# Kernel optimization log

Hardware: AMD Instinct MI355X
Metric: run time of the kernel (lower is better)

## Reference

```python
import jax, jax.numpy as jnp
import numpy as np
import itertools

N = 65536          # points
R = 1.0 / 16.0     # radius (forward uses 1/16)
K = 64             # max_num_neighbors in forward call
G = 16             # grid cells per axis (cell size == R)


def _radius_knn_edges(pts):
    """Grid-hashed radius search; per point keep nearest K within R (self-loop included),
    pad with self index so every point has exactly K edges (max-aggregation neutral)."""
    cells = np.minimum((pts / R).astype(np.int64), G - 1)
    cid = (cells[:, 0] * G + cells[:, 1]) * G + cells[:, 2]
    order = np.argsort(cid, kind='stable')
    sorted_cid = cid[order]
    counts = np.bincount(cid, minlength=G ** 3)
    starts = np.concatenate([[0], np.cumsum(counts)[:-1]])
    M = int(counts.max())
    cand = -np.ones((G ** 3, M), dtype=np.int64)
    slot = np.arange(N) - starts[sorted_cid]
    cand[sorted_cid, slot] = order
    offs = np.array(list(itertools.product([-1, 0, 1], repeat=3)))
    nbr = np.empty((N, K), dtype=np.int64)
    chunk = 4096
    for s in range(0, N, chunk):
        e = min(s + chunk, N)
        c = cells[s:e]
        nc = c[:, None, :] + offs[None]                      # [B,27,3]
        valid_c = np.all((nc >= 0) & (nc < G), axis=-1)      # [B,27]
        ncid = (nc[..., 0] * G + nc[..., 1]) * G + nc[..., 2]
        ncid = np.where(valid_c, ncid, 0)
        cd = cand[ncid]                                      # [B,27,M]
        cd = np.where(np.broadcast_to(valid_c[..., None], cd.shape), cd, -1)
        cd = cd.reshape(e - s, -1)                           # [B,27M]
        p = pts[np.maximum(cd, 0)]
        d = np.linalg.norm(p - pts[s:e, None, :], axis=-1)
        d = np.where((cd >= 0) & (d <= R), d, np.inf)
        sel = np.argsort(d, axis=1)[:, :K]
        row = np.arange(e - s)[:, None]
        picked = cd[row, sel]
        ok = np.isfinite(d[row, sel])
        nbr[s:e] = np.where(ok, picked, np.arange(s, e)[:, None])
    out_index = np.repeat(np.arange(N, dtype=np.int64), K)
    in_index = nbr.reshape(-1)
    return out_index, in_index


def setup_inputs() -> dict:
    key = jax.random.key(0)
    ks = jax.random.split(key, 16)
    pos = jax.random.uniform(ks[0], (N, 3), dtype=jnp.float32)
    rgb = jax.random.uniform(ks[1], (N, 3), dtype=jnp.float32)
    batch = jnp.zeros((N,), dtype=jnp.int64)
    oi, ii = _radius_knn_edges(np.asarray(pos, dtype=np.float64))
    out_index = jnp.asarray(oi)
    in_index = jnp.asarray(ii)

    def lin_w(k, fi, fo):
        return jax.random.normal(k, (fi, fo), dtype=jnp.float32) / np.sqrt(fi).astype(np.float32)

    def lin_b(k, fo):
        return 0.01 * jax.random.normal(k, (fo,), dtype=jnp.float32)

    return {
        'pos': pos, 'rgb': rgb, 'batch': batch,
        'out_index': out_index, 'in_index': in_index,
        'w1a': lin_w(ks[2], 6, 8),   'b1a': lin_b(ks[3], 8),
        'w1b': lin_w(ks[4], 8, 8),   'b1b': lin_b(ks[5], 8),
        'w2a': lin_w(ks[6], 11, 16), 'b2a': lin_b(ks[7], 16),
        'w2b': lin_w(ks[8], 16, 16), 'b2b': lin_b(ks[9], 16),
        'w3a': lin_w(ks[10], 19, 32), 'b3a': lin_b(ks[11], 32),
        'w3b': lin_w(ks[12], 32, 32), 'b3b': lin_b(ks[13], 32),
    }


def _point_conv(x, pos, out_index, in_index, wa, ba, wb, bb):
    # gather neighbor features + relative position, local MLP, max-scatter, output linear
    dpos = pos[in_index] - pos[out_index]                      # [E,3]
    msg = jnp.concatenate([x[in_index], dpos], axis=-1)        # [E,c_in+3]
    h = jax.nn.celu(msg @ wa + ba)                             # [E,c_mid]
    agg = jax.ops.segment_max(h, out_index, num_segments=pos.shape[0],
                              indices_are_sorted=True)         # [N,c_mid]
    return agg @ wb + bb                                       # [N,c_out]


def reference(pos, rgb, batch, out_index, in_index,
              w1a, b1a, w1b, b1b, w2a, b2a, w2b, b2b, w3a, b3a, w3b, b3b):
    out = jax.nn.celu(_point_conv(pos, pos, out_index, in_index, w1a, b1a, w1b, b1b))
    out = jax.nn.celu(_point_conv(out, pos, out_index, in_index, w2a, b2a, w2b, b2b))
    out = jax.nn.celu(_point_conv(out, pos, out_index, in_index, w3a, b3a, w3b, b3b))
    return (pos, out, batch)
```

## Files before the change

kernel.cpp:

```cpp
#include <hip/hip_runtime.h>
#include <hip/hip_fp16.h>
#include <math.h>


#define NPTS 65536
#define KNBR 64
#define TILE 32
#define NCELL 4096

__device__ __forceinline__ float celu1(float x) {
    return x > 0.0f ? x : (__expf(x) - 1.0f);
}

__device__ __forceinline__ unsigned pkmax(unsigned a, unsigned b) {
    unsigned d;
    asm("v_pk_max_f16 %0, %1, %2" : "=v"(d) : "v"(a), "v"(b));
    return d;
}

__device__ __forceinline__ unsigned pack2(float a, float b) {
    __half2 h = __floats2half2_rn(a, b);
    return *(unsigned*)&h;
}


__global__ __launch_bounds__(256) void k_cell(
    const float* __restrict__ pos, float* __restrict__ dout, int out_size,
    int* __restrict__ cid, int* __restrict__ hist)
{
    int t = blockIdx.x * 256 + threadIdx.x;
    if (t < NPTS) {
        float p0 = pos[3 * t + 0];
        float p1 = pos[3 * t + 1];
        float p2 = pos[3 * t + 2];
        dout[3 * t + 0] = p0;
        dout[3 * t + 1] = p1;
        dout[3 * t + 2] = p2;
        int cx = min((int)(p0 * 16.0f), 15);
        int cy = min((int)(p1 * 16.0f), 15);
        int cz = min((int)(p2 * 16.0f), 15);
        int c = (cx * 16 + cy) * 16 + cz;
        cid[t] = c;
        atomicAdd(&hist[c], 1);
        for (int j = 35 * NPTS + t; j < out_size; j += NPTS)
            dout[j] = 0.0f;
    }
}

__global__ __launch_bounds__(64) void k_scan(
    const int* __restrict__ hist, int* __restrict__ cellptr)
{
    int l = threadIdx.x;
    int v[64];
    int s = 0;
#pragma unroll
    for (int i = 0; i < 64; ++i) { v[i] = s; s += hist[l * 64 + i]; }
    int run = s;
#pragma unroll
    for (int st = 1; st < 64; st <<= 1) {
        int o = __shfl_up(run, st, 64);
        if (l >= st) run += o;
    }
    int off = run - s;
#pragma unroll
    for (int i = 0; i < 64; ++i)
        cellptr[l * 64 + i] = off + v[i];
}

__global__ __launch_bounds__(256) void k_scatter(
    const float* __restrict__ pos, const int* __restrict__ cid,
    int* __restrict__ cellptr, unsigned short* __restrict__ perm,
    int* __restrict__ order, float* __restrict__ pos_s,
    const float* __restrict__ w1a, const float* __restrict__ b1a,
    __half* __restrict__ q1s)
{
    int t = blockIdx.x * 256 + threadIdx.x;
    if (t >= NPTS) return;
    int c = cid[t];
    int nid = atomicAdd(&cellptr[c], 1);
    perm[t] = (unsigned short)nid;
    order[nid] = t;
    float p0 = pos[3 * t + 0];
    float p1 = pos[3 * t + 1];
    float p2 = pos[3 * t + 2];
    pos_s[3 * nid + 0] = p0;
    pos_s[3 * nid + 1] = p1;
    pos_s[3 * nid + 2] = p2;
    float q[8];
#pragma unroll
    for (int ch = 0; ch < 8; ++ch) {
        float a = b1a[ch];
        a = fmaf(p0, w1a[0 * 8 + ch] + w1a[3 * 8 + ch], a);
        a = fmaf(p1, w1a[1 * 8 + ch] + w1a[4 * 8 + ch], a);
        a = fmaf(p2, w1a[2 * 8 + ch] + w1a[5 * 8 + ch], a);
        q[ch] = a;
    }
    uint4 pk;
    pk.x = pack2(q[0], q[1]);
    pk.y = pack2(q[2], q[3]);
    pk.z = pack2(q[4], q[5]);
    pk.w = pack2(q[6], q[7]);
    *(uint4*)(q1s + 8 * nid) = pk;
}

__global__ __launch_bounds__(256) void k_trans(
    const int* __restrict__ idx, const int* __restrict__ order,
    const unsigned short* __restrict__ perm, unsigned short* __restrict__ idxs)
{
    int g = blockIdx.x * 256 + threadIdx.x;
    int row = g >> 3;
    int j = g & 7;
    int old = order[row];
    const int4* src = (const int4*)(idx + old * KNBR + j * 8);
    int4 v0 = src[0];
    int4 v1 = src[1];
    uint4 o;
    o.x = (unsigned)perm[v0.x] | ((unsigned)perm[v0.y] << 16);
    o.y = (unsigned)perm[v0.z] | ((unsigned)perm[v0.w] << 16);
    o.z = (unsigned)perm[v1.x] | ((unsigned)perm[v1.y] << 16);
    o.w = (unsigned)perm[v1.z] | ((unsigned)perm[v1.w] << 16);
    *(uint4*)(idxs + row * KNBR + j * 8) = o;
}

template <int FH, int FOUT, int FHN, bool WRITEX>
__global__ __launch_bounds__(256, 8) void k_layer(
    const __half* __restrict__ q,
    const unsigned short* __restrict__ idx,
    const float* __restrict__ pos,
    const int* __restrict__ order,
    const float* __restrict__ wap,
    const float* __restrict__ wb,
    const float* __restrict__ bb,
    const float* __restrict__ wan,
    const float* __restrict__ ban,
    float* __restrict__ xout,
    __half* __restrict__ qnext)
{
    constexpr int SL  = FH / 8;
    constexpr int LPP = SL * 8;
    constexpr int PPW = 64 / LPP;
    constexpr int NIT = TILE / (4 * PPW);

    __shared__ uint4 m_lds[TILE * SL];

    int w  = threadIdx.x >> 6;
    int l  = threadIdx.x & 63;
    int pl = l / LPP;
    int u  = l % LPP;
    int c  = u % SL;
    int g  = u / SL;
    int tb = (blockIdx.x & 255) * (NPTS / TILE / 256) + (blockIdx.x >> 8);
    int pbase = tb * TILE;

#pragma unroll
    for (int it = 0; it < NIT; ++it) {
        int lp = it * (4 * PPW) + w * PPW + pl;
        int p  = pbase + lp;
        uint4 iv = *(const uint4*)(idx + p * KNBR + g * 8);
        int e0 = iv.x & 0xffff, e1 = iv.x >> 16;
        int e2 = iv.y & 0xffff, e3 = iv.y >> 16;
        int e4 = iv.z & 0xffff, e5 = iv.z >> 16;
        int e6 = iv.w & 0xffff, e7 = iv.w >> 16;
        uint4 v[8];
        v[0] = *(const uint4*)(q + e0 * FH + c * 8);
        v[1] = *(const uint4*)(q + e1 * FH + c * 8);
        v[2] = *(const uint4*)(q + e2 * FH + c * 8);
        v[3] = *(const uint4*)(q + e3 * FH + c * 8);
        v[4] = *(const uint4*)(q + e4 * FH + c * 8);
        v[5] = *(const uint4*)(q + e5 * FH + c * 8);
        v[6] = *(const uint4*)(q + e6 * FH + c * 8);
        v[7] = *(const uint4*)(q + e7 * FH + c * 8);

        unsigned ax = 0xFC00FC00u, ay = 0xFC00FC00u, az = 0xFC00FC00u, aw = 0xFC00FC00u;
#pragma unroll
        for (int k = 0; k < 8; ++k) {
            ax = pkmax(ax, v[k].x);
            ay = pkmax(ay, v[k].y);
            az = pkmax(az, v[k].z);
            aw = pkmax(aw, v[k].w);
        }
#pragma unroll
        for (int st = SL; st < LPP; st <<= 1) {
            ax = pkmax(ax, (unsigned)__shfl_xor((int)ax, st, 64));
            ay = pkmax(ay, (unsigned)__shfl_xor((int)ay, st, 64));
            az = pkmax(az, (unsigned)__shfl_xor((int)az, st, 64));
            aw = pkmax(aw, (unsigned)__shfl_xor((int)aw, st, 64));
        }
        if (g == 0) {
            uint4 r; r.x = ax; r.y = ay; r.z = az; r.w = aw;
            m_lds[lp * SL + c] = r;
        }
    }
    __syncthreads();

    if constexpr (WRITEX) {
        if (threadIdx.x < TILE * 4) {
            int pt  = threadIdx.x >> 2;
            int qtr = threadIdx.x & 3;
            int p   = pbase + pt;
            float p0 = pos[3 * p + 0];
            float p1 = pos[3 * p + 1];
            float p2 = pos[3 * p + 2];

            float h[FH];
#pragma unroll
            for (int s = 0; s < SL; ++s) {
                uint4 vv = m_lds[pt * SL + s];
                unsigned w4[4] = {vv.x, vv.y, vv.z, vv.w};
#pragma unroll
                for (int k = 0; k < 4; ++k) {
                    float2 f = __half22float2(*(__half2*)&w4[k]);
                    h[s * 8 + k * 2 + 0] = f.x;
                    h[s * 8 + k * 2 + 1] = f.y;
                }
            }
#pragma unroll
            for (int ch = 0; ch < FH; ++ch) {
                float gg = p0 * wap[ch] + p1 * wap[FH + ch] + p2 * wap[2 * FH + ch];
                h[ch] = celu1(h[ch] - gg);
            }
            float x[8];
#pragma unroll
            for (int j = 0; j < 8; ++j) {
                int c2 = qtr * 8 + j;
                float a = bb[c2];
#pragma unroll
                for (int ch = 0; ch < FH; ++ch)
                    a = fmaf(h[ch], wb[ch * FOUT + c2], a);
                x[j] = celu1(a);
            }
            int oldp = order[p];
            float4* xo = (float4*)(xout + (long long)oldp * FOUT + qtr * 8);
            xo[0] = make_float4(x[0], x[1], x[2], x[3]);
            xo[1] = make_float4(x[4], x[5], x[6], x[7]);
        }
    } else if (threadIdx.x < TILE) {
        int lt = threadIdx.x;
        int p  = pbase + lt;
        float p0 = pos[3 * p + 0];
        float p1 = pos[3 * p + 1];
        float p2 = pos[3 * p + 2];

        float h[FH];
#pragma unroll
        for (int s = 0; s < SL; ++s) {
            uint4 vv = m_lds[lt * SL + s];
            unsigned w4[4] = {vv.x, vv.y, vv.z, vv.w};
#pragma unroll
            for (int k = 0; k < 4; ++k) {
                float2 f = __half22float2(*(__half2*)&w4[k]);
                h[s * 8 + k * 2 + 0] = f.x;
                h[s * 8 + k * 2 + 1] = f.y;
            }
        }
#pragma unroll
        for (int ch = 0; ch < FH; ++ch) {
            float gg = p0 * wap[ch] + p1 * wap[FH + ch] + p2 * wap[2 * FH + ch];
            h[ch] = celu1(h[ch] - gg);
        }
        float x[FOUT];
#pragma unroll
        for (int c2 = 0; c2 < FOUT; ++c2) {
            float a = bb[c2];
#pragma unroll
            for (int ch = 0; ch < FH; ++ch)
                a = fmaf(h[ch], wb[ch * FOUT + c2], a);
            x[c2] = celu1(a);
        }
        if constexpr (FHN > 0) {
            uint4* qo = (uint4*)(qnext + p * FHN);
#pragma unroll
            for (int s = 0; s < FHN / 8; ++s) {
                float qn[8];
#pragma unroll
                for (int k = 0; k < 8; ++k) {
                    int cn = s * 8 + k;
                    float a = ban[cn];
#pragma unroll
                    for (int c2 = 0; c2 < FOUT; ++c2)
                        a = fmaf(x[c2], wan[c2 * FHN + cn], a);
                    a = fmaf(p0, wan[(FOUT + 0) * FHN + cn], a);
                    a = fmaf(p1, wan[(FOUT + 1) * FHN + cn], a);
                    a = fmaf(p2, wan[(FOUT + 2) * FHN + cn], a);
                    qn[k] = a;
                }
                uint4 pk;
                pk.x = pack2(qn[0], qn[1]);
                pk.y = pack2(qn[2], qn[3]);
                pk.z = pack2(qn[4], qn[5]);
                pk.w = pack2(qn[6], qn[7]);
                qo[s] = pk;
            }
        }
    }
}

extern "C" void kernel_launch(void* const* d_in, const int* in_sizes, int n_in,
                              void* d_out, int out_size, void* d_ws, size_t ws_size,
                              hipStream_t stream) {
    const float* pos = (const float*)d_in[0];
    const int* idx = (const int*)d_in[4];
    const float* w1a = (const float*)d_in[5];
    const float* b1a = (const float*)d_in[6];
    const float* w1b = (const float*)d_in[7];
    const float* b1b = (const float*)d_in[8];
    const float* w2a = (const float*)d_in[9];
    const float* b2a = (const float*)d_in[10];
    const float* w2b = (const float*)d_in[11];
    const float* b2b = (const float*)d_in[12];
    const float* w3a = (const float*)d_in[13];
    const float* b3a = (const float*)d_in[14];
    const float* w3b = (const float*)d_in[15];
    const float* b3b = (const float*)d_in[16];
    float* out = (float*)d_out;

    char* ws = (char*)d_ws;
    __half* A      = (__half*)ws;
    __half* B      = (__half*)(ws + (4u << 20));
    unsigned short* idxs = (unsigned short*)(ws + (6u << 20));
    int*    cid    = (int*)(ws + (14u << 20));
    int*    order  = (int*)(ws + (14u << 20) + (256u << 10));
    unsigned short* perm = (unsigned short*)(ws + (14u << 20) + (512u << 10));
    int*    hist   = (int*)(ws + (14u << 20) + (640u << 10));
    int*    cellptr= (int*)(ws + (14u << 20) + (656u << 10));
    float*  pos_s  = (float*)(ws + (15u << 20));

    hipMemsetAsync(hist, 0, NCELL * sizeof(int), stream);
    k_cell<<<NPTS / 256, 256, 0, stream>>>(pos, out, out_size, cid, hist);
    k_scan<<<1, 64, 0, stream>>>(hist, cellptr);
    k_scatter<<<NPTS / 256, 256, 0, stream>>>(pos, cid, cellptr, perm, order,
                                              pos_s, w1a, b1a, A);
    k_trans<<<NPTS * 8 / 256, 256, 0, stream>>>(idx, order, perm, idxs);

    k_layer<8, 8, 16, false><<<NPTS / TILE, 256, 0, stream>>>(
        A, idxs, pos_s, nullptr, w1a + 3 * 8, w1b, b1b, w2a, b2a, nullptr, B);
    k_layer<16, 16, 32, false><<<NPTS / TILE, 256, 0, stream>>>(
        B, idxs, pos_s, nullptr, w2a + 8 * 16, w2b, b2b, w3a, b3a, nullptr, A);
    k_layer<32, 32, 0, true><<<NPTS / TILE, 256, 0, stream>>>(
        A, idxs, pos_s, order, w3a + 16 * 32, w3b, b3b, nullptr, nullptr,
        out + 3 * NPTS, nullptr);
}
```

Before: 176.5 us.

## Fuse neighbor index transform into first layer and parallelize epilogue across threads

Removes the separate k_trans kernel and folds the order/perm remapping of neighbor indices into the first layer's gather loop, which also writes the 16-bit sorted index table for later layers. The non-WRITEX epilogue now splits each point's output channels and next-layer projection over 2 or 4 threads, staged through shared memory with a barrier, instead of using only 32 threads. This cuts a kernel launch and an extra pass over the index array and raises epilogue parallelism, at the cost of extra LDS use and a __syncthreads in every block.

```diff
diff --git a/kernel.cpp b/kernel.cpp
--- a/kernel.cpp
+++ b/kernel.cpp
@@ -103,29 +103,13 @@
     *(uint4*)(q1s + 8 * nid) = pk;
 }
 
-__global__ __launch_bounds__(256) void k_trans(
-    const int* __restrict__ idx, const int* __restrict__ order,
-    const unsigned short* __restrict__ perm, unsigned short* __restrict__ idxs)
-{
-    int g = blockIdx.x * 256 + threadIdx.x;
-    int row = g >> 3;
-    int j = g & 7;
-    int old = order[row];
-    const int4* src = (const int4*)(idx + old * KNBR + j * 8);
-    int4 v0 = src[0];
-    int4 v1 = src[1];
-    uint4 o;
-    o.x = (unsigned)perm[v0.x] | ((unsigned)perm[v0.y] << 16);
-    o.y = (unsigned)perm[v0.z] | ((unsigned)perm[v0.w] << 16);
-    o.z = (unsigned)perm[v1.x] | ((unsigned)perm[v1.y] << 16);
-    o.w = (unsigned)perm[v1.z] | ((unsigned)perm[v1.w] << 16);
-    *(uint4*)(idxs + row * KNBR + j * 8) = o;
-}
-
-template <int FH, int FOUT, int FHN, bool WRITEX>
+template <int FH, int FOUT, int FHN, bool WRITEX, bool FUSE>
 __global__ __launch_bounds__(256, 8) void k_layer(
     const __half* __restrict__ q,
     const unsigned short* __restrict__ idx,
+    const int* __restrict__ idx_old,
+    unsigned short* __restrict__ idxs_out,
+    const unsigned short* __restrict__ perm,
     const float* __restrict__ pos,
     const int* __restrict__ order,
     const float* __restrict__ wap,
@@ -140,8 +124,10 @@
     constexpr int LPP = SL * 8;
     constexpr int PPW = 64 / LPP;
     constexpr int NIT = TILE / (4 * PPW);
+    constexpr int QW  = (FOUT >= 16) ? 4 : 2;
 
     __shared__ uint4 m_lds[TILE * SL];
+    __shared__ float x_lds[(FHN > 0) ? TILE * (FOUT + 1) : 1];
 
     int w  = threadIdx.x >> 6;
     int l  = threadIdx.x & 63;
@@ -156,11 +142,27 @@
     for (int it = 0; it < NIT; ++it) {
         int lp = it * (4 * PPW) + w * PPW + pl;
         int p  = pbase + lp;
-        uint4 iv = *(const uint4*)(idx + p * KNBR + g * 8);
-        int e0 = iv.x & 0xffff, e1 = iv.x >> 16;
-        int e2 = iv.y & 0xffff, e3 = iv.y >> 16;
-        int e4 = iv.z & 0xffff, e5 = iv.z >> 16;
-        int e6 = iv.w & 0xffff, e7 = iv.w >> 16;
+        int e0, e1, e2, e3, e4, e5, e6, e7;
+        if constexpr (FUSE) {
+            int old = order[p];
+            const int4* src = (const int4*)(idx_old + old * KNBR + g * 8);
+            int4 v0 = src[0];
+            int4 v1 = src[1];
+            e0 = perm[v0.x]; e1 = perm[v0.y]; e2 = perm[v0.z]; e3 = perm[v0.w];
+            e4 = perm[v1.x]; e5 = perm[v1.y]; e6 = perm[v1.z]; e7 = perm[v1.w];
+            uint4 o;
+            o.x = (unsigned)e0 | ((unsigned)e1 << 16);
+            o.y = (unsigned)e2 | ((unsigned)e3 << 16);
+            o.z = (unsigned)e4 | ((unsigned)e5 << 16);
+            o.w = (unsigned)e6 | ((unsigned)e7 << 16);
+            *(uint4*)(idxs_out + p * KNBR + g * 8) = o;
+        } else {
+            uint4 iv = *(const uint4*)(idx + p * KNBR + g * 8);
+            e0 = iv.x & 0xffff; e1 = iv.x >> 16;
+            e2 = iv.y & 0xffff; e3 = iv.y >> 16;
+            e4 = iv.z & 0xffff; e5 = iv.z >> 16;
+            e6 = iv.w & 0xffff; e7 = iv.w >> 16;
+        }
         uint4 v[8];
         v[0] = *(const uint4*)(q + e0 * FH + c * 8);
         v[1] = *(const uint4*)(q + e1 * FH + c * 8);
@@ -234,47 +236,55 @@
             xo[0] = make_float4(x[0], x[1], x[2], x[3]);
             xo[1] = make_float4(x[4], x[5], x[6], x[7]);
         }
-    } else if (threadIdx.x < TILE) {
-        int lt = threadIdx.x;
-        int p  = pbase + lt;
-        float p0 = pos[3 * p + 0];
-        float p1 = pos[3 * p + 1];
-        float p2 = pos[3 * p + 2];
-
-        float h[FH];
-#pragma unroll
-        for (int s = 0; s < SL; ++s) {
-            uint4 vv = m_lds[lt * SL + s];
-            unsigned w4[4] = {vv.x, vv.y, vv.z, vv.w};
-#pragma unroll
-            for (int k = 0; k < 4; ++k) {
-                float2 f = __half22float2(*(__half2*)&w4[k]);
-                h[s * 8 + k * 2 + 0] = f.x;
-                h[s * 8 + k * 2 + 1] = f.y;
-            }
-        }
-#pragma unroll
-        for (int ch = 0; ch < FH; ++ch) {
-            float gg = p0 * wap[ch] + p1 * wap[FH + ch] + p2 * wap[2 * FH + ch];
-            h[ch] = celu1(h[ch] - gg);
-        }
-        float x[FOUT];
-#pragma unroll
-        for (int c2 = 0; c2 < FOUT; ++c2) {
-            float a = bb[c2];
-#pragma unroll
-            for (int ch = 0; ch < FH; ++ch)
-                a = fmaf(h[ch], wb[ch * FOUT + c2], a);
-            x[c2] = celu1(a);
-        }
+    } else {
+        constexpr int XS = FOUT / QW;
+        float p0 = 0.f, p1 = 0.f, p2 = 0.f;
+        int pt = threadIdx.x / QW;
+        int qq = threadIdx.x % QW;
+        if (threadIdx.x < TILE * QW) {
+            int p = pbase + pt;
+            p0 = pos[3 * p + 0];
+            p1 = pos[3 * p + 1];
+            p2 = pos[3 * p + 2];
+            float h[FH];
+#pragma unroll
+            for (int s = 0; s < SL; ++s) {
+                uint4 vv = m_lds[pt * SL + s];
+                unsigned w4[4] = {vv.x, vv.y, vv.z, vv.w};
+#pragma unroll
+                for (int k = 0; k < 4; ++k) {
+                    float2 f = __half22float2(*(__half2*)&w4[k]);
+                    h[s * 8 + k * 2 + 0] = f.x;
+                    h[s * 8 + k * 2 + 1] = f.y;
+                }
+            }
+#pragma unroll
+            for (int ch = 0; ch < FH; ++ch) {
+                float gg = p0 * wap[ch] + p1 * wap[FH + ch] + p2 * wap[2 * FH + ch];
+                h[ch] = celu1(h[ch] - gg);
+            }
+#pragma unroll
+            for (int j = 0; j < XS; ++j) {
+                int c2 = qq * XS + j;
+                float a = bb[c2];
+#pragma unroll
+                for (int ch = 0; ch < FH; ++ch)
+                    a = fmaf(h[ch], wb[ch * FOUT + c2], a);
+                x_lds[pt * (FOUT + 1) + c2] = celu1(a);
+            }
+        }
+        __syncthreads();
         if constexpr (FHN > 0) {
-            uint4* qo = (uint4*)(qnext + p * FHN);
-#pragma unroll
-            for (int s = 0; s < FHN / 8; ++s) {
+            if (threadIdx.x < TILE * QW) {
+                int p = pbase + pt;
+                float x[FOUT];
+#pragma unroll
+                for (int c2 = 0; c2 < FOUT; ++c2)
+                    x[c2] = x_lds[pt * (FOUT + 1) + c2];
                 float qn[8];
 #pragma unroll
                 for (int k = 0; k < 8; ++k) {
-                    int cn = s * 8 + k;
+                    int cn = qq * 8 + k;
                     float a = ban[cn];
 #pragma unroll
                     for (int c2 = 0; c2 < FOUT; ++c2)
@@ -289,7 +299,7 @@
                 pk.y = pack2(qn[2], qn[3]);
                 pk.z = pack2(qn[4], qn[5]);
                 pk.w = pack2(qn[6], qn[7]);
-                qo[s] = pk;
+                *(uint4*)(qnext + p * FHN + qq * 8) = pk;
             }
         }
     }
@@ -330,13 +340,14 @@
     k_scan<<<1, 64, 0, stream>>>(hist, cellptr);
     k_scatter<<<NPTS / 256, 256, 0, stream>>>(pos, cid, cellptr, perm, order,
                                               pos_s, w1a, b1a, A);
-    k_trans<<<NPTS * 8 / 256, 256, 0, stream>>>(idx, order, perm, idxs);
-
-    k_layer<8, 8, 16, false><<<NPTS / TILE, 256, 0, stream>>>(
-        A, idxs, pos_s, nullptr, w1a + 3 * 8, w1b, b1b, w2a, b2a, nullptr, B);
-    k_layer<16, 16, 32, false><<<NPTS / TILE, 256, 0, stream>>>(
-        B, idxs, pos_s, nullptr, w2a + 8 * 16, w2b, b2b, w3a, b3a, nullptr, A);
-    k_layer<32, 32, 0, true><<<NPTS / TILE, 256, 0, stream>>>(
-        A, idxs, pos_s, order, w3a + 16 * 32, w3b, b3b, nullptr, nullptr,
-        out + 3 * NPTS, nullptr);
-}
+
+    k_layer<8, 8, 16, false, true><<<NPTS / TILE, 256, 0, stream>>>(
+        A, nullptr, idx, idxs, perm, pos_s, order,
+        w1a + 3 * 8, w1b, b1b, w2a, b2a, nullptr, B);
+    k_layer<16, 16, 32, false, false><<<NPTS / TILE, 256, 0, stream>>>(
+        B, idxs, nullptr, nullptr, nullptr, pos_s, nullptr,
+        w2a + 8 * 16, w2b, b2b, w3a, b3a, nullptr, A);
+    k_layer<32, 32, 0, true, false><<<NPTS / TILE, 256, 0, stream>>>(
+        A, idxs, nullptr, nullptr, nullptr, pos_s, order,
+        w3a + 16 * 32, w3b, b3b, nullptr, nullptr, out + 3 * NPTS, nullptr);
+}
```

Result: no change. 178.4 us (+1.1%).
